# Kernel tuning notes

Measured on AMD Instinct MI355X. Metric: run time of the kernel, lower is better.

Reference implementation:

```python
import jax, jax.numpy as jnp
import numpy as np

B, L, D = 1, 2048, 4096
H, KV, HD = 32, 8, 128
ROT = 64  # head_dim * partial_rotary_factor
SCALE = HD ** -0.5
NEG = -1e9


def _apply_rope(x, cos, sin):
    # x: [B, h, L, HD]; rotate only the first ROT dims (partial rotary, rotate-half convention)
    xr, xp = x[..., :ROT], x[..., ROT:]
    x1, x2 = jnp.split(xr, 2, axis=-1)
    rotated = jnp.concatenate([-x2, x1], axis=-1)
    xr = xr * cos[None, None] + rotated * sin[None, None]
    return jnp.concatenate([xr, xp], axis=-1)


def setup_inputs() -> dict:
    key = jax.random.key(0)
    k1, k2, k3 = jax.random.split(key, 3)
    x = jax.random.normal(k1, (B, L, D), jnp.float32)
    w_qkv = jax.random.normal(k2, (D, H * HD + 2 * KV * HD), jnp.float32) * 0.02
    w_o = jax.random.normal(k3, (H * HD, D), jnp.float32) * 0.02
    # causal additive mask, broadcast over batch and heads
    causal = jnp.tril(jnp.ones((L, L), dtype=bool))
    attention_mask = jnp.where(causal, 0.0, NEG).astype(jnp.float32)[None, None]
    # rotary tables over the ROT rotary dims
    inv_freq = 1.0 / (10000.0 ** (jnp.arange(0, ROT, 2, dtype=jnp.float32) / ROT))
    t = jnp.arange(L, dtype=jnp.float32)
    freqs = jnp.outer(t, inv_freq)            # [L, ROT/2]
    emb = jnp.concatenate([freqs, freqs], -1)  # [L, ROT]
    cos, sin = jnp.cos(emb), jnp.sin(emb)
    return {"x": x, "attention_mask": attention_mask, "cos": cos, "sin": sin,
            "w_qkv": w_qkv, "w_o": w_o}


def reference(x, attention_mask, cos, sin, w_qkv, w_o):
    Bx, Lx, _ = x.shape
    qkv = x @ w_qkv                                   # [B, L, H*HD + 2*KV*HD]
    q_pos = H * HD
    kv_pos = q_pos + KV * HD
    q = qkv[:, :, :q_pos].reshape(Bx, Lx, H, HD).transpose(0, 2, 1, 3)
    k = qkv[:, :, q_pos:kv_pos].reshape(Bx, Lx, KV, HD).transpose(0, 2, 1, 3)
    v = qkv[:, :, kv_pos:].reshape(Bx, Lx, KV, HD).transpose(0, 2, 1, 3)
    q = _apply_rope(q, cos, sin)
    k = _apply_rope(k, cos, sin)
    # GQA: duplicate KV heads (as in the original module)
    n_rep = H // KV
    k = jnp.repeat(k, n_rep, axis=1)
    v = jnp.repeat(v, n_rep, axis=1)
    w = jnp.einsum("bhqd,bhkd->bhqk", q, k) * SCALE   # [B, H, L, L]
    w = jax.nn.softmax(w + attention_mask, axis=-1)
    o = jnp.einsum("bhqk,bhkd->bhqd", w, v)           # [B, H, L, HD]
    o = o.transpose(0, 2, 1, 3).reshape(Bx, Lx, H * HD)
    return o @ w_o
```

## Files before the change

### kernel.cpp

```cpp
#include <hip/hip_runtime.h>
#include <stdint.h>

typedef float f32x4 __attribute__((ext_vector_type(4)));
typedef short s16x8 __attribute__((ext_vector_type(8)));
typedef unsigned short u16x4 __attribute__((ext_vector_type(4)));
typedef unsigned short u16x8 __attribute__((ext_vector_type(8)));

#define SCALE_F 0.08838834764831845f

__device__ __forceinline__ unsigned short f32_to_bf16(float f) {
    union { float f; unsigned int u; } v; v.f = f;
    return (unsigned short)((v.u + 0x7FFFu + ((v.u >> 16) & 1u)) >> 16);
}
__device__ __forceinline__ float bf16_to_f32(unsigned short h) {
    union { unsigned int u; float f; } v; v.u = (unsigned int)h << 16;
    return v.f;
}

__device__ __forceinline__ void gload16(const void* g, void* l) {
    __builtin_amdgcn_global_load_lds((const __attribute__((address_space(1))) unsigned int*)g,
                                     (__attribute__((address_space(3))) unsigned int*)l,
                                     16, 0, 0);
}

__global__ void k_conv_bf16(const float* __restrict__ in, unsigned short* __restrict__ out, int n4) {
    int i = blockIdx.x * 256 + threadIdx.x;
    if (i >= n4) return;
    f32x4 v = ((const f32x4*)in)[i];
    u16x4 o;
    o[0] = f32_to_bf16(v[0]); o[1] = f32_to_bf16(v[1]);
    o[2] = f32_to_bf16(v[2]); o[3] = f32_to_bf16(v[3]);
    ((u16x4*)out)[i] = o;
}

__global__ void k_transpose_f32(const float* __restrict__ in, unsigned short* __restrict__ out,
                                int R, int in_ld, int in_off) {
    __shared__ float tile[64][65];
    const int rb = blockIdx.y * 64, cb = blockIdx.x * 64;
    const int t = threadIdx.x;
    const int lr = t >> 4, lc4 = (t & 15) * 4;
#pragma unroll
    for (int i = 0; i < 4; ++i) {
        int r = i * 16 + lr;
        f32x4 v = *(const f32x4*)(in + (size_t)(rb + r) * in_ld + in_off + cb + lc4);
        tile[r][lc4 + 0] = v[0]; tile[r][lc4 + 1] = v[1];
        tile[r][lc4 + 2] = v[2]; tile[r][lc4 + 3] = v[3];
    }
    __syncthreads();
#pragma unroll
    for (int i = 0; i < 4; ++i) {
        int oc = cb + i * 16 + lr;
        u16x4 o;
#pragma unroll
        for (int j = 0; j < 4; ++j)
            o[j] = f32_to_bf16(tile[lc4 + j][i * 16 + lr]);
        *(u16x4*)(out + (size_t)oc * R + rb + lc4) = o;
    }
}

__global__ void k_transpose_b16(const unsigned short* __restrict__ in, unsigned short* __restrict__ out,
                                int R, int in_ld, int in_off) {
    __shared__ unsigned short tile[64][68];
    const int rb = blockIdx.y * 64, cb = blockIdx.x * 64;
    const int t = threadIdx.x;
    const int lr = t >> 4, lc4 = (t & 15) * 4;
#pragma unroll
    for (int i = 0; i < 4; ++i) {
        int r = i * 16 + lr;
        u16x4 v = *(const u16x4*)(in + (size_t)(rb + r) * in_ld + in_off + cb + lc4);
        tile[r][lc4 + 0] = v[0]; tile[r][lc4 + 1] = v[1];
        tile[r][lc4 + 2] = v[2]; tile[r][lc4 + 3] = v[3];
    }
    __syncthreads();
#pragma unroll
    for (int i = 0; i < 4; ++i) {
        int oc = cb + i * 16 + lr;
        u16x4 o;
#pragma unroll
        for (int j = 0; j < 4; ++j)
            o[j] = tile[lc4 + j][i * 16 + lr];
        *(u16x4*)(out + (size_t)oc * R + rb + lc4) = o;
    }
}

__global__ __launch_bounds__(512, 1)
void k_gemmA(const unsigned short* __restrict__ A, const unsigned short* __restrict__ Bt,
             unsigned short* __restrict__ C, int N, int K) {
    __shared__ __align__(16) unsigned short As[2][2][4096];
    __shared__ __align__(16) unsigned short Bs[2][2][12288];
    const int tid = threadIdx.x;
    const int lane = tid & 63, wid = tid >> 6;
    const int g = lane >> 4, l15 = lane & 15;
    const int wm = wid >> 2, wn = wid & 3;
    const int nwg = gridDim.x, bid = blockIdx.x;
    const int swz = (bid & 7) * (nwg >> 3) + (bid >> 3);
    const int bn = swz >> 4, bm = swz & 15;
    const int brow = bm << 7, bcol = bn * 384;

    const int rS = tid >> 2;
    const int kcS = (tid & 3) ^ (rS & 3) ^ ((rS >> 2) & 3);
    const unsigned short* sA = A + (size_t)(brow + rS) * K + kcS * 8;
    const unsigned short* sB = Bt + (size_t)(bcol + rS) * K + kcS * 8;
    const int fsw = (g ^ (l15 & 3) ^ ((l15 >> 2) & 3)) * 8;

    f32x4 acc[4][6] = {};
    const int nt = K >> 6;

    auto stA = [&](int t, int kh) {
        unsigned short* d = &As[t & 1][kh][tid * 8];
        gload16(sA + (size_t)t * 64 + kh * 32, d);
    };
    auto stB = [&](int t, int kh) {
        unsigned short* d = &Bs[t & 1][kh][tid * 8];
        const unsigned short* s = sB + (size_t)t * 64 + kh * 32;
        gload16(s, d);
        gload16(s + (size_t)128 * K, d + 4096);
        gload16(s + (size_t)256 * K, d + 8192);
    };

    stA(0, 0); stB(0, 0); stA(0, 1); stB(0, 1);

    for (int t = 0; t < nt; ++t) {
        const int c = t & 1;
#pragma unroll
        for (int kh = 0; kh < 2; ++kh) {
            if (t + 1 < nt)   { stA(t + 1, kh); stB(t + 1, kh); asm volatile("s_waitcnt vmcnt(8)" ::: "memory"); }
            else if (kh == 0) { asm volatile("s_waitcnt vmcnt(4)" ::: "memory"); }
            else              { asm volatile("s_waitcnt vmcnt(0)" ::: "memory"); }
            __builtin_amdgcn_s_barrier();
            s16x8 af[4], bf[6];
#pragma unroll
            for (int f = 0; f < 4; ++f)
                af[f] = *(const s16x8*)(&As[c][kh][(wm * 64 + f * 16 + l15) * 32 + fsw]);
#pragma unroll
            for (int j = 0; j < 6; ++j)
                bf[j] = *(const s16x8*)(&Bs[c][kh][(wn * 96 + j * 16 + l15) * 32 + fsw]);
            __builtin_amdgcn_s_setprio(1);
#pragma unroll
            for (int f = 0; f < 4; ++f)
#pragma unroll
                for (int j = 0; j < 6; ++j)
                    acc[f][j] = __builtin_amdgcn_mfma_f32_16x16x32_bf16(af[f], bf[j], acc[f][j], 0, 0, 0);
            __builtin_amdgcn_s_setprio(0);
        }
    }

#pragma unroll
    for (int f = 0; f < 4; ++f)
#pragma unroll
        for (int j = 0; j < 6; ++j)
#pragma unroll
            for (int r = 0; r < 4; ++r)
                C[(size_t)(brow + wm * 64 + f * 16 + g * 4 + r) * N
                  + bcol + wn * 96 + j * 16 + l15] = f32_to_bf16(acc[f][j][r]);
}

__global__ __launch_bounds__(512, 1)
void k_gemmB(const unsigned short* __restrict__ A, const unsigned short* __restrict__ Bt,
             float* __restrict__ C, int N, int K) {
    __shared__ __align__(16) unsigned short As[2][2][4096];
    __shared__ __align__(16) unsigned short Bs[2][2][8192];
    const int tid = threadIdx.x;
    const int lane = tid & 63, wid = tid >> 6;
    const int g = lane >> 4, l15 = lane & 15;
    const int wm = wid >> 2, wn = wid & 3;
    const int nwg = gridDim.x, bid = blockIdx.x;
    const int swz = (bid & 7) * (nwg >> 3) + (bid >> 3);
    const int bn = swz >> 4, bm = swz & 15;
    const int brow = bm << 7, bcol = bn << 8;

    const int rS = tid >> 2;
    const int kcS = (tid & 3) ^ (rS & 3) ^ ((rS >> 2) & 3);
    const unsigned short* sA = A + (size_t)(brow + rS) * K + kcS * 8;
    const unsigned short* sB = Bt + (size_t)(bcol + rS) * K + kcS * 8;
    const int fsw = (g ^ (l15 & 3) ^ ((l15 >> 2) & 3)) * 8;

    f32x4 acc[4][4] = {};
    const int nt = K >> 6;

    auto stA = [&](int t, int kh) {
        gload16(sA + (size_t)t * 64 + kh * 32, &As[t & 1][kh][tid * 8]);
    };
    auto stB = [&](int t, int kh) {
        unsigned short* d = &Bs[t & 1][kh][tid * 8];
        const unsigned short* s = sB + (size_t)t * 64 + kh * 32;
        gload16(s, d);
        gload16(s + (size_t)128 * K, d + 4096);
    };

    stA(0, 0); stB(0, 0); stA(0, 1); stB(0, 1);

    for (int t = 0; t < nt; ++t) {
        const int c = t & 1;
#pragma unroll
        for (int kh = 0; kh < 2; ++kh) {
            if (t + 1 < nt) { stA(t + 1, kh); stB(t + 1, kh); asm volatile("s_waitcnt vmcnt(6)" ::: "memory"); }
            else if (kh == 0) { asm volatile("s_waitcnt vmcnt(3)" ::: "memory"); }
            else              { asm volatile("s_waitcnt vmcnt(0)" ::: "memory"); }
            __builtin_amdgcn_s_barrier();
            s16x8 af[4], bf[4];
#pragma unroll
            for (int f = 0; f < 4; ++f)
                af[f] = *(const s16x8*)(&As[c][kh][(wm * 64 + f * 16 + l15) * 32 + fsw]);
#pragma unroll
            for (int j = 0; j < 4; ++j)
                bf[j] = *(const s16x8*)(&Bs[c][kh][(wn * 64 + j * 16 + l15) * 32 + fsw]);
            __builtin_amdgcn_s_setprio(1);
#pragma unroll
            for (int f = 0; f < 4; ++f)
#pragma unroll
                for (int j = 0; j < 4; ++j)
                    acc[f][j] = __builtin_amdgcn_mfma_f32_16x16x32_bf16(af[f], bf[j], acc[f][j], 0, 0, 0);
            __builtin_amdgcn_s_setprio(0);
        }
    }

#pragma unroll
    for (int f = 0; f < 4; ++f)
#pragma unroll
        for (int j = 0; j < 4; ++j)
#pragma unroll
            for (int r = 0; r < 4; ++r)
                C[(size_t)(brow + wm * 64 + f * 16 + g * 4 + r) * N
                  + bcol + wn * 64 + j * 16 + l15] = acc[f][j][r];
}

__global__ void k_rope_pack(const unsigned short* __restrict__ qkv, const float* __restrict__ cosT,
                            const float* __restrict__ sinT, unsigned short* __restrict__ Qb,
                            unsigned short* __restrict__ Kb) {
    const int oct = blockIdx.x * 128 + threadIdx.x;
    if (oct >= 640) return;
    const int col = oct * 8;
    const int t = blockIdx.y;
    const int d = col & 127;
    const bool isQ = (col < 4096);
    const float post = isQ ? SCALE_F : 1.0f;
    u16x8 v8 = *(const u16x8*)(qkv + (size_t)t * 6144 + col);
    u16x8 o8;
    if (d < 64) {
        u16x8 p8 = *(const u16x8*)(qkv + (size_t)t * 6144 + (col ^ 32));
        f32x4 c0 = *(const f32x4*)(cosT + t * 64 + d);
        f32x4 c1 = *(const f32x4*)(cosT + t * 64 + d + 4);
        f32x4 s0 = *(const f32x4*)(sinT + t * 64 + d);
        f32x4 s1 = *(const f32x4*)(sinT + t * 64 + d + 4);
        const float sgn = (d < 32) ? -1.f : 1.f;
#pragma unroll
        for (int j = 0; j < 8; ++j) {
            float cc = (j < 4) ? c0[j] : c1[j - 4];
            float ss = (j < 4) ? s0[j] : s1[j - 4];
            float o = (bf16_to_f32(v8[j]) * cc + sgn * bf16_to_f32(p8[j]) * ss) * post;
            o8[j] = f32_to_bf16(o);
        }
    } else {
#pragma unroll
        for (int j = 0; j < 8; ++j)
            o8[j] = f32_to_bf16(bf16_to_f32(v8[j]) * post);
    }
    if (isQ) {
        const int h = col >> 7;
        *(u16x8*)(Qb + ((size_t)h * 2048 + t) * 128 + d) = o8;
    } else {
        const int hk = (col - 4096) >> 7;
        *(u16x8*)(Kb + ((size_t)hk * 2048 + t) * 128 + d) = o8;
    }
}

__global__ __launch_bounds__(256, 2)
void k_attn(const unsigned short* __restrict__ Qb, const unsigned short* __restrict__ Kb,
            const unsigned short* __restrict__ Vt, unsigned short* __restrict__ Ob) {
    __shared__ __align__(16) unsigned short Ks[2][8192];
    __shared__ __align__(16) unsigned short Vs[2][8192];
    __shared__ __align__(16) unsigned short Pl[2][4][1024];
    const int h = blockIdx.y, hk = h >> 2;
    const int qbA = blockIdx.x, qbB = 31 - qbA;
    const int tid = threadIdx.x, lane = tid & 63, wid = tid >> 6;
    const int g = lane >> 4, l15 = lane & 15;
    const int qrA = qbA * 64 + wid * 16, qrB = qbB * 64 + wid * 16;
    const int swz = (l15 & 7) << 4;

    s16x8 aqA[4], aqB[4];
#pragma unroll
    for (int kc = 0; kc < 4; ++kc) {
        aqA[kc] = *(const s16x8*)(Qb + ((size_t)h * 2048 + qrA + l15) * 128 + kc * 32 + g * 8);
        aqB[kc] = *(const s16x8*)(Qb + ((size_t)h * 2048 + qrB + l15) * 128 + kc * 32 + g * 8);
    }

    const unsigned short* gK = Kb + ((size_t)hk * 2048 + (tid & 63)) * 128 + (tid >> 6) * 8;
    const unsigned short* gV = Vt + ((size_t)hk * 128 + (tid & 127)) * 2048 + (tid >> 7) * 8;

    auto stage = [&](int kb) {
        unsigned short* dK = Ks[kb & 1] + tid * 8;
        unsigned short* dV = Vs[kb & 1] + tid * 8;
        const unsigned short* sK = gK + (size_t)kb * 8192;
        const unsigned short* sV = gV + kb * 64;
#pragma unroll
        for (int i = 0; i < 4; ++i) gload16(sK + i * 32, dK + i * 2048);
#pragma unroll
        for (int i = 0; i < 4; ++i) gload16(sV + i * 16, dV + i * 2048);
    };

    f32x4 oaccA[8] = {}, oaccB[8] = {};
    float mA = -1e30f, lA = 0.f, mB = -1e30f, lB = 0.f;

    auto sm = [&](f32x4* s, f32x4* oacc, float& mr, float& lr, int qrow0, int kb, char* pw) {
        const int q = qrow0 + l15;
        if (kb * 64 + 63 > qrow0) {
#pragma unroll
            for (int kt = 0; kt < 4; ++kt)
#pragma unroll
                for (int r = 0; r < 4; ++r)
                    if (kb * 64 + kt * 16 + g * 4 + r > q) s[kt][r] = -3e38f;
        }
        float mx = -3e38f;
#pragma unroll
        for (int kt = 0; kt < 4; ++kt)
#pragma unroll
            for (int r = 0; r < 4; ++r) mx = fmaxf(mx, s[kt][r]);
        mx = fmaxf(mx, __shfl_xor(mx, 16));
        mx = fmaxf(mx, __shfl_xor(mx, 32));
        if (!__all(mx - mr <= 8.0f)) {
            const float mnew = fmaxf(mr, mx);
            const float scal = __expf(mr - mnew);
            mr = mnew;
            float so[4];
#pragma unroll
            for (int r = 0; r < 4; ++r) so[r] = __shfl(scal, g * 4 + r, 16);
#pragma unroll
            for (int j = 0; j < 8; ++j) {
                oacc[j][0] *= so[0]; oacc[j][1] *= so[1];
                oacc[j][2] *= so[2]; oacc[j][3] *= so[3];
            }
            lr *= scal;
        }
        float ps = 0.f;
#pragma unroll
        for (int kt = 0; kt < 4; ++kt)
#pragma unroll
            for (int r = 0; r < 4; ++r) {
                float p = __expf(s[kt][r] - mr);
                s[kt][r] = p;
                ps += p;
            }
        ps += __shfl_xor(ps, 16);
        ps += __shfl_xor(ps, 32);
        lr += ps;
#pragma unroll
        for (int kt = 0; kt < 4; ++kt) {
            unsigned int w0 = (unsigned int)f32_to_bf16(s[kt][0]) | ((unsigned int)f32_to_bf16(s[kt][1]) << 16);
            unsigned int w1 = (unsigned int)f32_to_bf16(s[kt][2]) | ((unsigned int)f32_to_bf16(s[kt][3]) << 16);
            const int b0 = (l15 * 128 + kt * 32 + g * 8) ^ swz;
            *(unsigned int*)(pw + b0) = w0;
            *(unsigned int*)(pw + b0 + 4) = w1;
        }
    };

    const int nkb = qbB + 1;
    stage(0);
    for (int kb = 0; kb < nkb; ++kb) {
        if (kb + 1 < nkb) {
            stage(kb + 1);
            asm volatile("s_waitcnt vmcnt(8)" ::: "memory");
        } else {
            asm volatile("s_waitcnt vmcnt(0)" ::: "memory");
        }
        __builtin_amdgcn_s_barrier();
        const unsigned short* ks = Ks[kb & 1];
        const unsigned short* vs = Vs[kb & 1];
        char* pwA = (char*)Pl[0][wid];
        char* pwB = (char*)Pl[1][wid];
        const bool doA = (kb <= qbA);
        f32x4 sB_[4] = {}, sA_[4] = {};
        __builtin_amdgcn_s_setprio(1);
        if (doA) {
#pragma unroll
            for (int kc = 0; kc < 4; ++kc)
#pragma unroll
                for (int kt = 0; kt < 4; ++kt) {
                    s16x8 kf = *(const s16x8*)(ks + ((kc * 4 + g) * 64 + kt * 16 + l15) * 8);
                    sB_[kt] = __builtin_amdgcn_mfma_f32_16x16x32_bf16(kf, aqB[kc], sB_[kt], 0, 0, 0);
                    sA_[kt] = __builtin_amdgcn_mfma_f32_16x16x32_bf16(kf, aqA[kc], sA_[kt], 0, 0, 0);
                }
        } else {
#pragma unroll
            for (int kc = 0; kc < 4; ++kc)
#pragma unroll
                for (int kt = 0; kt < 4; ++kt) {
                    s16x8 kf = *(const s16x8*)(ks + ((kc * 4 + g) * 64 + kt * 16 + l15) * 8);
                    sB_[kt] = __builtin_amdgcn_mfma_f32_16x16x32_bf16(kf, aqB[kc], sB_[kt], 0, 0, 0);
                }
        }
        __builtin_amdgcn_s_setprio(0);
        sm(sB_, oaccB, mB, lB, qrB, kb, pwB);
        if (doA) sm(sA_, oaccA, mA, lA, qrA, kb, pwA);
        __builtin_amdgcn_s_setprio(1);
        if (doA) {
#pragma unroll
            for (int kc = 0; kc < 2; ++kc) {
                s16x8 paB = *(const s16x8*)(pwB + ((l15 * 128 + kc * 64 + g * 16) ^ swz));
                s16x8 paA = *(const s16x8*)(pwA + ((l15 * 128 + kc * 64 + g * 16) ^ swz));
#pragma unroll
                for (int j = 0; j < 8; ++j) {
                    s16x8 bv = *(const s16x8*)(vs + ((kc * 4 + g) * 128 + j * 16 + l15) * 8);
                    oaccB[j] = __builtin_amdgcn_mfma_f32_16x16x32_bf16(paB, bv, oaccB[j], 0, 0, 0);
                    oaccA[j] = __builtin_amdgcn_mfma_f32_16x16x32_bf16(paA, bv, oaccA[j], 0, 0, 0);
                }
            }
        } else {
#pragma unroll
            for (int kc = 0; kc < 2; ++kc) {
                s16x8 paB = *(const s16x8*)(pwB + ((l15 * 128 + kc * 64 + g * 16) ^ swz));
#pragma unroll
                for (int j = 0; j < 8; ++j) {
                    s16x8 bv = *(const s16x8*)(vs + ((kc * 4 + g) * 128 + j * 16 + l15) * 8);
                    oaccB[j] = __builtin_amdgcn_mfma_f32_16x16x32_bf16(paB, bv, oaccB[j], 0, 0, 0);
                }
            }
        }
        __builtin_amdgcn_s_setprio(0);
        __builtin_amdgcn_s_barrier();
    }
    float liA[4], liB[4];
#pragma unroll
    for (int r = 0; r < 4; ++r) {
        liA[r] = 1.f / __shfl(lA, g * 4 + r, 16);
        liB[r] = 1.f / __shfl(lB, g * 4 + r, 16);
    }
#pragma unroll
    for (int j = 0; j < 8; ++j)
#pragma unroll
        for (int r = 0; r < 4; ++r) {
            Ob[(size_t)(qrA + g * 4 + r) * 4096 + h * 128 + j * 16 + l15] = f32_to_bf16(oaccA[j][r] * liA[r]);
            Ob[(size_t)(qrB + g * 4 + r) * 4096 + h * 128 + j * 16 + l15] = f32_to_bf16(oaccB[j][r] * liB[r]);
        }
}

extern "C" void kernel_launch(void* const* d_in, const int* in_sizes, int n_in,
                              void* d_out, int out_size, void* d_ws, size_t ws_size,
                              hipStream_t stream) {
    const float* x     = (const float*)d_in[0];
    const float* cosT  = (const float*)d_in[2];
    const float* sinT  = (const float*)d_in[3];
    const float* w_qkv = (const float*)d_in[4];
    const float* w_o   = (const float*)d_in[5];
    float* out = (float*)d_out;

    char* ws = (char*)d_ws;
    unsigned short* wT   = (unsigned short*)(ws + 0);
    unsigned short* qkvb = (unsigned short*)(ws + 50331648);
    unsigned short* Ob   = (unsigned short*)(ws + 50331648);
    unsigned short* xb   = (unsigned short*)(ws + 100663296);
    unsigned short* Qb   = xb;
    unsigned short* Kb   = (unsigned short*)(ws + 117440512);
    unsigned short* Vt   = (unsigned short*)(ws + 121634816);

    k_conv_bf16<<<8192, 256, 0, stream>>>(x, xb, 2097152);
    k_transpose_f32<<<dim3(96, 64), 256, 0, stream>>>(w_qkv, wT, 4096, 6144, 0);
    k_gemmA<<<256, 512, 0, stream>>>(xb, wT, qkvb, 6144, 4096);
    k_rope_pack<<<dim3(5, 2048), 128, 0, stream>>>(qkvb, cosT, sinT, Qb, Kb);
    k_transpose_b16<<<dim3(16, 32), 256, 0, stream>>>(qkvb, Vt, 2048, 6144, 5120);
    k_transpose_f32<<<dim3(64, 64), 256, 0, stream>>>(w_o, wT, 4096, 4096, 0);
    k_attn<<<dim3(16, 32), 256, 0, stream>>>(Qb, Kb, Vt, Ob);
    k_gemmB<<<256, 512, 0, stream>>>(Ob, wT, out, 4096, 4096);
}
```

Baseline: 353.9 us.

## Merge attention work groups into 512-thread blocks sharing K/V tiles across four query blocks

The attention kernel now runs 512 threads per block. Each block covers four causal query blocks (two mirrored pairs) of one head, where before it covered two, and the grid halves from 16x32 to 8x32. Each K/V tile is staged once in shared memory and reused by all eight waves, which halves global K/V traffic per query row. The cost is fewer, larger blocks: 256 blocks with one per CU, more barrier-coupled waves, and waves that sit idle once their query blocks pass the causal limit.

```diff
diff --git a/kernel.cpp b/kernel.cpp
--- a/kernel.cpp
+++ b/kernel.cpp
@@ -107,8 +107,7 @@
     const int nt = K >> 6;
 
     auto stA = [&](int t, int kh) {
-        unsigned short* d = &As[t & 1][kh][tid * 8];
-        gload16(sA + (size_t)t * 64 + kh * 32, d);
+        gload16(sA + (size_t)t * 64 + kh * 32, &As[t & 1][kh][tid * 8]);
     };
     auto stB = [&](int t, int kh) {
         unsigned short* d = &Bs[t & 1][kh][tid * 8];
@@ -265,24 +264,27 @@
     }
 }
 
-__global__ __launch_bounds__(256, 2)
+__global__ __launch_bounds__(512, 1)
 void k_attn(const unsigned short* __restrict__ Qb, const unsigned short* __restrict__ Kb,
             const unsigned short* __restrict__ Vt, unsigned short* __restrict__ Ob) {
     __shared__ __align__(16) unsigned short Ks[2][8192];
     __shared__ __align__(16) unsigned short Vs[2][8192];
-    __shared__ __align__(16) unsigned short Pl[2][4][1024];
+    __shared__ __align__(16) unsigned short Pl[8][2][1024];
     const int h = blockIdx.y, hk = h >> 2;
-    const int qbA = blockIdx.x, qbB = 31 - qbA;
+    const int bid = blockIdx.x;
     const int tid = threadIdx.x, lane = tid & 63, wid = tid >> 6;
     const int g = lane >> 4, l15 = lane & 15;
-    const int qrA = qbA * 64 + wid * 16, qrB = qbB * 64 + wid * 16;
+    const int sl = (wid & 3) * 16;
+    const int qb0 = (wid < 4) ? bid : bid + 8;
+    const int qb1 = (wid < 4) ? 31 - bid : 23 - bid;
+    const int qr0 = qb0 * 64 + sl, qr1 = qb1 * 64 + sl;
     const int swz = (l15 & 7) << 4;
 
-    s16x8 aqA[4], aqB[4];
+    s16x8 aq0[4], aq1[4];
 #pragma unroll
     for (int kc = 0; kc < 4; ++kc) {
-        aqA[kc] = *(const s16x8*)(Qb + ((size_t)h * 2048 + qrA + l15) * 128 + kc * 32 + g * 8);
-        aqB[kc] = *(const s16x8*)(Qb + ((size_t)h * 2048 + qrB + l15) * 128 + kc * 32 + g * 8);
+        aq0[kc] = *(const s16x8*)(Qb + ((size_t)h * 2048 + qr0 + l15) * 128 + kc * 32 + g * 8);
+        aq1[kc] = *(const s16x8*)(Qb + ((size_t)h * 2048 + qr1 + l15) * 128 + kc * 32 + g * 8);
     }
 
     const unsigned short* gK = Kb + ((size_t)hk * 2048 + (tid & 63)) * 128 + (tid >> 6) * 8;
@@ -294,13 +296,13 @@
         const unsigned short* sK = gK + (size_t)kb * 8192;
         const unsigned short* sV = gV + kb * 64;
 #pragma unroll
-        for (int i = 0; i < 4; ++i) gload16(sK + i * 32, dK + i * 2048);
-#pragma unroll
-        for (int i = 0; i < 4; ++i) gload16(sV + i * 16, dV + i * 2048);
-    };
-
-    f32x4 oaccA[8] = {}, oaccB[8] = {};
-    float mA = -1e30f, lA = 0.f, mB = -1e30f, lB = 0.f;
+        for (int i = 0; i < 2; ++i) gload16(sK + i * 64, dK + i * 4096);
+#pragma unroll
+        for (int i = 0; i < 2; ++i) gload16(sV + i * 32, dV + i * 4096);
+    };
+
+    f32x4 oacc0[8] = {}, oacc1[8] = {};
+    float m0 = -1e30f, l0 = 0.f, m1 = -1e30f, l1 = 0.f;
 
     auto sm = [&](f32x4* s, f32x4* oacc, float& mr, float& lr, int qrow0, int kb, char* pw) {
         const int q = qrow0 + l15;
@@ -354,83 +356,86 @@
         }
     };
 
-    const int nkb = qbB + 1;
+    const int nkb = 32 - bid;
     stage(0);
     for (int kb = 0; kb < nkb; ++kb) {
         if (kb + 1 < nkb) {
             stage(kb + 1);
-            asm volatile("s_waitcnt vmcnt(8)" ::: "memory");
+            asm volatile("s_waitcnt vmcnt(4)" ::: "memory");
         } else {
             asm volatile("s_waitcnt vmcnt(0)" ::: "memory");
         }
         __builtin_amdgcn_s_barrier();
         const unsigned short* ks = Ks[kb & 1];
         const unsigned short* vs = Vs[kb & 1];
-        char* pwA = (char*)Pl[0][wid];
-        char* pwB = (char*)Pl[1][wid];
-        const bool doA = (kb <= qbA);
-        f32x4 sB_[4] = {}, sA_[4] = {};
-        __builtin_amdgcn_s_setprio(1);
-        if (doA) {
-#pragma unroll
-            for (int kc = 0; kc < 4; ++kc)
-#pragma unroll
-                for (int kt = 0; kt < 4; ++kt) {
-                    s16x8 kf = *(const s16x8*)(ks + ((kc * 4 + g) * 64 + kt * 16 + l15) * 8);
-                    sB_[kt] = __builtin_amdgcn_mfma_f32_16x16x32_bf16(kf, aqB[kc], sB_[kt], 0, 0, 0);
-                    sA_[kt] = __builtin_amdgcn_mfma_f32_16x16x32_bf16(kf, aqA[kc], sA_[kt], 0, 0, 0);
+        char* pw0 = (char*)Pl[wid][0];
+        char* pw1 = (char*)Pl[wid][1];
+        const bool a0 = (kb <= qb0);
+        const bool a1 = (kb <= qb1);
+        f32x4 s0_[4] = {}, s1_[4] = {};
+        if (a1) {
+            __builtin_amdgcn_s_setprio(1);
+            if (a0) {
+#pragma unroll
+                for (int kc = 0; kc < 4; ++kc)
+#pragma unroll
+                    for (int kt = 0; kt < 4; ++kt) {
+                        s16x8 kf = *(const s16x8*)(ks + ((kc * 4 + g) * 64 + kt * 16 + l15) * 8);
+                        s1_[kt] = __builtin_amdgcn_mfma_f32_16x16x32_bf16(kf, aq1[kc], s1_[kt], 0, 0, 0);
+                        s0_[kt] = __builtin_amdgcn_mfma_f32_16x16x32_bf16(kf, aq0[kc], s0_[kt], 0, 0, 0);
+                    }
+            } else {
+#pragma unroll
+                for (int kc = 0; kc < 4; ++kc)
+#pragma unroll
+                    for (int kt = 0; kt < 4; ++kt) {
+                        s16x8 kf = *(const s16x8*)(ks + ((kc * 4 + g) * 64 + kt * 16 + l15) * 8);
+                        s1_[kt] = __builtin_amdgcn_mfma_f32_16x16x32_bf16(kf, aq1[kc], s1_[kt], 0, 0, 0);
+                    }
+            }
+            __builtin_amdgcn_s_setprio(0);
+            sm(s1_, oacc1, m1, l1, qr1, kb, pw1);
+            if (a0) sm(s0_, oacc0, m0, l0, qr0, kb, pw0);
+            __builtin_amdgcn_s_setprio(1);
+            if (a0) {
+#pragma unroll
+                for (int kc = 0; kc < 2; ++kc) {
+                    s16x8 pa1 = *(const s16x8*)(pw1 + ((l15 * 128 + kc * 64 + g * 16) ^ swz));
+                    s16x8 pa0 = *(const s16x8*)(pw0 + ((l15 * 128 + kc * 64 + g * 16) ^ swz));
+#pragma unroll
+                    for (int j = 0; j < 8; ++j) {
+                        s16x8 bv = *(const s16x8*)(vs + ((kc * 4 + g) * 128 + j * 16 + l15) * 8);
+                        oacc1[j] = __builtin_amdgcn_mfma_f32_16x16x32_bf16(pa1, bv, oacc1[j], 0, 0, 0);
+                        oacc0[j] = __builtin_amdgcn_mfma_f32_16x16x32_bf16(pa0, bv, oacc0[j], 0, 0, 0);
+                    }
                 }
-        } else {
-#pragma unroll
-            for (int kc = 0; kc < 4; ++kc)
-#pragma unroll
-                for (int kt = 0; kt < 4; ++kt) {
-                    s16x8 kf = *(const s16x8*)(ks + ((kc * 4 + g) * 64 + kt * 16 + l15) * 8);
-                    sB_[kt] = __builtin_amdgcn_mfma_f32_16x16x32_bf16(kf, aqB[kc], sB_[kt], 0, 0, 0);
-                }
-        }
-        __builtin_amdgcn_s_setprio(0);
-        sm(sB_, oaccB, mB, lB, qrB, kb, pwB);
-        if (doA) sm(sA_, oaccA, mA, lA, qrA, kb, pwA);
-        __builtin_amdgcn_s_setprio(1);
-        if (doA) {
-#pragma unroll
-            for (int kc = 0; kc < 2; ++kc) {
-                s16x8 paB = *(const s16x8*)(pwB + ((l15 * 128 + kc * 64 + g * 16) ^ swz));
-                s16x8 paA = *(const s16x8*)(pwA + ((l15 * 128 + kc * 64 + g * 16) ^ swz));
-#pragma unroll
-                for (int j = 0; j < 8; ++j) {
-                    s16x8 bv = *(const s16x8*)(vs + ((kc * 4 + g) * 128 + j * 16 + l15) * 8);
-                    oaccB[j] = __builtin_amdgcn_mfma_f32_16x16x32_bf16(paB, bv, oaccB[j], 0, 0, 0);
-                    oaccA[j] = __builtin_amdgcn_mfma_f32_16x16x32_bf16(paA, bv, oaccA[j], 0, 0, 0);
+            } else {
+#pragma unroll
+                for (int kc = 0; kc < 2; ++kc) {
+                    s16x8 pa1 = *(const s16x8*)(pw1 + ((l15 * 128 + kc * 64 + g * 16) ^ swz));
+#pragma unroll
+                    for (int j = 0; j < 8; ++j) {
+                        s16x8 bv = *(const s16x8*)(vs + ((kc * 4 + g) * 128 + j * 16 + l15) * 8);
+                        oacc1[j] = __builtin_amdgcn_mfma_f32_16x16x32_bf16(pa1, bv, oacc1[j], 0, 0, 0);
+                    }
                 }
             }
-        } else {
-#pragma unroll
-            for (int kc = 0; kc < 2; ++kc) {
-                s16x8 paB = *(const s16x8*)(pwB + ((l15 * 128 + kc * 64 + g * 16) ^ swz));
-#pragma unroll
-                for (int j = 0; j < 8; ++j) {
-                    s16x8 bv = *(const s16x8*)(vs + ((kc * 4 + g) * 128 + j * 16 + l15) * 8);
-                    oaccB[j] = __builtin_amdgcn_mfma_f32_16x16x32_bf16(paB, bv, oaccB[j], 0, 0, 0);
-                }
-            }
-        }
-        __builtin_amdgcn_s_setprio(0);
+            __builtin_amdgcn_s_setprio(0);
+        }
         __builtin_amdgcn_s_barrier();
     }
-    float liA[4], liB[4];
+    float li0[4], li1[4];
 #pragma unroll
     for (int r = 0; r < 4; ++r) {
-        liA[r] = 1.f / __shfl(lA, g * 4 + r, 16);
-        liB[r] = 1.f / __shfl(lB, g * 4 + r, 16);
+        li0[r] = 1.f / __shfl(l0, g * 4 + r, 16);
+        li1[r] = 1.f / __shfl(l1, g * 4 + r, 16);
     }
 #pragma unroll
     for (int j = 0; j < 8; ++j)
 #pragma unroll
         for (int r = 0; r < 4; ++r) {
-            Ob[(size_t)(qrA + g * 4 + r) * 4096 + h * 128 + j * 16 + l15] = f32_to_bf16(oaccA[j][r] * liA[r]);
-            Ob[(size_t)(qrB + g * 4 + r) * 4096 + h * 128 + j * 16 + l15] = f32_to_bf16(oaccB[j][r] * liB[r]);
+            Ob[(size_t)(qr0 + g * 4 + r) * 4096 + h * 128 + j * 16 + l15] = f32_to_bf16(oacc0[j][r] * li0[r]);
+            Ob[(size_t)(qr1 + g * 4 + r) * 4096 + h * 128 + j * 16 + l15] = f32_to_bf16(oacc1[j][r] * li1[r]);
         }
 }
 
@@ -459,6 +464,6 @@
     k_rope_pack<<<dim3(5, 2048), 128, 0, stream>>>(qkvb, cosT, sinT, Qb, Kb);
     k_transpose_b16<<<dim3(16, 32), 256, 0, stream>>>(qkvb, Vt, 2048, 6144, 5120);
     k_transpose_f32<<<dim3(64, 64), 256, 0, stream>>>(w_o, wT, 4096, 4096, 0);
-    k_attn<<<dim3(16, 32), 256, 0, stream>>>(Qb, Kb, Vt, Ob);
+    k_attn<<<dim3(8, 32), 512, 0, stream>>>(Qb, Kb, Vt, Ob);
     k_gemmB<<<256, 512, 0, stream>>>(Ob, wT, out, 4096, 4096);
 }
```

Result: no change. 355.7 us (+0.5%).
